# Optimization experiments

Hardware: AMD Instinct MI355X
Metric: run time of the kernel (lower is better)

## Reference

```python
import jax, jax.numpy as jnp
import numpy as np

B, S, D, H = 4, 2048, 1024, 16
HD = D // H  # head dim = 64


def setup_inputs() -> dict:
    key = jax.random.key(0)
    ks = jax.random.split(key, 9)
    scale = 1.0 / np.sqrt(D)
    return {
        "x": jax.random.normal(ks[0], (B, S, D), dtype=jnp.float32),
        "Wq": jax.random.normal(ks[1], (D, D), dtype=jnp.float32) * scale,
        "bq": jnp.zeros((D,), dtype=jnp.float32),
        "Wk": jax.random.normal(ks[2], (D, D), dtype=jnp.float32) * scale,
        "bk": jnp.zeros((D,), dtype=jnp.float32),
        "Wv": jax.random.normal(ks[3], (D, D), dtype=jnp.float32) * scale,
        "bv": jnp.zeros((D,), dtype=jnp.float32),
        "Wo": jax.random.normal(ks[4], (D, D), dtype=jnp.float32) * scale,
        "bo": jnp.zeros((D,), dtype=jnp.float32),
    }


def _split_heads(t):
    # [B,S,D] -> [B,H,S,HD]
    return t.reshape(t.shape[0], t.shape[1], H, HD).transpose(0, 2, 1, 3)


def reference(x, Wq, bq, Wk, bk, Wv, bv, Wo, bo):
    q = _split_heads(x @ Wq + bq)
    k = _split_heads(x @ Wk + bk)
    v = _split_heads(x @ Wv + bv)
    # scaled dot-product attention; scale by sqrt of key dim (= head dim)
    scores = jnp.einsum("bhqd,bhkd->bhqk", q, k) / jnp.sqrt(jnp.asarray(HD, q.dtype))
    weights = jax.nn.softmax(scores, axis=-1)
    attn = jnp.einsum("bhqk,bhkd->bhqd", weights, v)
    concat = attn.transpose(0, 2, 1, 3).reshape(x.shape[0], -1, D)
    out = concat @ Wo + bo
    return out, weights
```

## Files before the change

### kernel.cpp

```cpp
#include <hip/hip_runtime.h>
#include <cstddef>
#include <cstdint>

static constexpr int BB = 4;
static constexpr int SS = 2048;
static constexpr int DD = 1024;
static constexpr int HH = 16;
static constexpr int HDIM = 64;
static constexpr int MROWS = BB * SS;

typedef __attribute__((ext_vector_type(4))) float f32x4;
typedef __bf16 bf16x8 __attribute__((ext_vector_type(8)));
typedef __bf16 bf16x4 __attribute__((ext_vector_type(4)));

#define GLB_U32(p) ((const __attribute__((address_space(1))) uint32_t*)(p))
#define LDS_U32(p) ((__attribute__((address_space(3))) uint32_t*)(p))

__device__ __forceinline__ float fexp2(float x) {
#if __has_builtin(__builtin_amdgcn_exp2f)
    return __builtin_amdgcn_exp2f(x);
#else
    return exp2f(x);
#endif
}

__global__ __launch_bounds__(256) void cvt_x(const float* __restrict__ x,
                                             __bf16* __restrict__ xb)
{
    size_t i = ((size_t)blockIdx.x * 256 + threadIdx.x) * 8;
    float4 a = *reinterpret_cast<const float4*>(x + i);
    float4 b = *reinterpret_cast<const float4*>(x + i + 4);
    bf16x8 v;
    v[0] = (__bf16)a.x; v[1] = (__bf16)a.y; v[2] = (__bf16)a.z; v[3] = (__bf16)a.w;
    v[4] = (__bf16)b.x; v[5] = (__bf16)b.y; v[6] = (__bf16)b.z; v[7] = (__bf16)b.w;
    *reinterpret_cast<bf16x8*>(xb + i) = v;
}

__global__ __launch_bounds__(256) void transpose_w(
    const float* __restrict__ W0, const float* __restrict__ W1,
    const float* __restrict__ W2, const float* __restrict__ W3,
    __bf16* __restrict__ wt_base)
{
    const float* W = (blockIdx.z == 0) ? W0 : (blockIdx.z == 1) ? W1
                   : (blockIdx.z == 2) ? W2 : W3;
    __bf16* WT = wt_base + (size_t)blockIdx.z * 1048576;

    __shared__ float T[64][68];
    const int t = threadIdx.x;
    const int n0 = blockIdx.x * 64, k0 = blockIdx.y * 64;

#pragma unroll
    for (int it = 0; it < 4; ++it) {
        const int row = it * 16 + (t >> 4);
        const int col = (t & 15) * 4;
        float4 v = *reinterpret_cast<const float4*>(&W[(size_t)(k0 + row) * 1024 + n0 + col]);
        T[row][col + 0] = v.x; T[row][col + 1] = v.y;
        T[row][col + 2] = v.z; T[row][col + 3] = v.w;
    }
    __syncthreads();

#pragma unroll
    for (int it = 0; it < 2; ++it) {
        const int idx = it * 256 + t;
        const int n = idx >> 3, ch = idx & 7;
        bf16x8 v;
#pragma unroll
        for (int e = 0; e < 8; ++e) v[e] = (__bf16)T[ch * 8 + e][n];
        *reinterpret_cast<bf16x8*>(&WT[(size_t)(n0 + n) * 1024 + k0 + ch * 8]) = v;
    }
}

__global__ __launch_bounds__(256) void gemm_qkv(
    const __bf16* __restrict__ xb, const __bf16* __restrict__ wt,
    const float* __restrict__ bq, const float* __restrict__ bk,
    const float* __restrict__ bv,
    __bf16* __restrict__ qb, __bf16* __restrict__ kb, __bf16* __restrict__ vtb)
{
    __shared__ __bf16 AB[2 * 128 * 32];
    __bf16* At = AB;
    __bf16* Bt = AB + 4096;

    const int t = threadIdx.x;
    const int w = t >> 6, l = t & 63, l16 = l & 15, lg = l >> 4;
    const int m0 = blockIdx.x * 128;
    const int sel = blockIdx.y >> 3;
    const int n0 = (blockIdx.y & 7) * 128;
    const int wr = w >> 1, wc = w & 1;

    const __bf16* BT = wt + (size_t)sel * 1048576;
    const float* bias = (sel == 0) ? bq : (sel == 1) ? bk : bv;

    f32x4 acc[4][4] = {};

    for (int k0 = 0; k0 < 1024; k0 += 32) {
#pragma unroll
        for (int r = 0; r < 2; ++r) {
            const int cb = (w * 2 + r) * 64;
            const int ch = cb + l;
            const __bf16* srcA = xb + (size_t)(m0 + (ch >> 2)) * 1024 + k0 + (ch & 3) * 8;
            __builtin_amdgcn_global_load_lds(GLB_U32(srcA), LDS_U32(At + cb * 8), 16, 0, 0);
        }
#pragma unroll
        for (int r = 0; r < 2; ++r) {
            const int cb = (w * 2 + r) * 64;
            const int ch = cb + l;
            const __bf16* srcB = BT + (size_t)(n0 + (ch >> 2)) * 1024 + k0 + (ch & 3) * 8;
            __builtin_amdgcn_global_load_lds(GLB_U32(srcB), LDS_U32(Bt + cb * 8), 16, 0, 0);
        }
        __syncthreads();

        bf16x8 af[4], bf[4];
#pragma unroll
        for (int i = 0; i < 4; ++i) {
            af[i] = *reinterpret_cast<const bf16x8*>(At + (wr * 64 + i * 16 + l16) * 32 + lg * 8);
            bf[i] = *reinterpret_cast<const bf16x8*>(Bt + (wc * 64 + i * 16 + l16) * 32 + lg * 8);
        }
#pragma unroll
        for (int i = 0; i < 4; ++i)
#pragma unroll
            for (int j = 0; j < 4; ++j)
                acc[i][j] = __builtin_amdgcn_mfma_f32_16x16x32_bf16(af[i], bf[j], acc[i][j], 0, 0, 0);
        __syncthreads();
    }

    const float osc = (sel == 0) ? 0.18033688011112042f : 1.0f;

    if (sel < 2) {
        __bf16* Et = AB + w * 2048;
        __bf16* outp = (sel == 0) ? qb : kb;
#pragma unroll
        for (int j = 0; j < 4; ++j) {
            const float bvv = bias[n0 + wc * 64 + j * 16 + l16];
#pragma unroll
            for (int i = 0; i < 4; ++i)
#pragma unroll
                for (int r = 0; r < 4; ++r)
                    Et[(i * 16 + lg * 4 + r) * 24 + l16] =
                        (__bf16)((acc[i][j][r] + bvv) * osc);
#pragma unroll
            for (int it = 0; it < 2; ++it) {
                const int idx = it * 64 + l;
                const int ml = idx >> 1, ch = idx & 1;
                bf16x8 v = *(const bf16x8*)(Et + ml * 24 + ch * 8);
                const int M = m0 + wr * 64 + ml;
                const int N = n0 + wc * 64 + j * 16 + ch * 8;
                *(bf16x8*)(outp + (((size_t)(M >> 11) * HH + (N >> 6)) * SS
                                   + (M & 2047)) * HDIM + (N & 63)) = v;
            }
        }
    } else {
        __bf16* Et = AB + w * 2048;
#pragma unroll
        for (int j = 0; j < 4; ++j) {
            const float bvv = bias[n0 + wc * 64 + j * 16 + l16];
#pragma unroll
            for (int i = 0; i < 4; ++i)
#pragma unroll
                for (int r = 0; r < 4; ++r)
                    Et[l16 * 72 + i * 16 + lg * 4 + r] = (__bf16)(acc[i][j][r] + bvv);
#pragma unroll
            for (int it = 0; it < 2; ++it) {
                const int idx = it * 64 + l;
                const int row = idx >> 3, ch = idx & 7;
                bf16x8 v = *(const bf16x8*)(Et + row * 72 + ch * 8);
                const int N = n0 + wc * 64 + j * 16 + row;
                const int M = m0 + wr * 64 + ch * 8;
                *(bf16x8*)(vtb + (((size_t)(M >> 11) * HH + (N >> 6)) * HDIM
                                  + (N & 63)) * SS + (M & 2047)) = v;
            }
        }
    }
}

__global__ __launch_bounds__(256) void gemm_out(
    const __bf16* __restrict__ A, const __bf16* __restrict__ BT,
    const float* __restrict__ bias, float* __restrict__ C)
{
    __shared__ __bf16 AB[2 * 128 * 32];
    __bf16* At = AB;
    __bf16* Bt = AB + 4096;

    const int t = threadIdx.x;
    const int w = t >> 6, l = t & 63, l16 = l & 15, lg = l >> 4;
    const int m0 = blockIdx.x * 128, n0 = blockIdx.y * 128;
    const int wr = w >> 1, wc = w & 1;

    f32x4 acc[4][4] = {};

    for (int k0 = 0; k0 < 1024; k0 += 32) {
#pragma unroll
        for (int r = 0; r < 2; ++r) {
            const int cb = (w * 2 + r) * 64;
            const int ch = cb + l;
            const __bf16* srcA = A + (size_t)(m0 + (ch >> 2)) * 1024 + k0 + (ch & 3) * 8;
            __builtin_amdgcn_global_load_lds(GLB_U32(srcA), LDS_U32(At + cb * 8), 16, 0, 0);
        }
#pragma unroll
        for (int r = 0; r < 2; ++r) {
            const int cb = (w * 2 + r) * 64;
            const int ch = cb + l;
            const __bf16* srcB = BT + (size_t)(n0 + (ch >> 2)) * 1024 + k0 + (ch & 3) * 8;
            __builtin_amdgcn_global_load_lds(GLB_U32(srcB), LDS_U32(Bt + cb * 8), 16, 0, 0);
        }
        __syncthreads();

        bf16x8 af[4], bf[4];
#pragma unroll
        for (int i = 0; i < 4; ++i) {
            af[i] = *reinterpret_cast<const bf16x8*>(At + (wr * 64 + i * 16 + l16) * 32 + lg * 8);
            bf[i] = *reinterpret_cast<const bf16x8*>(Bt + (wc * 64 + i * 16 + l16) * 32 + lg * 8);
        }
#pragma unroll
        for (int i = 0; i < 4; ++i)
#pragma unroll
            for (int j = 0; j < 4; ++j)
                acc[i][j] = __builtin_amdgcn_mfma_f32_16x16x32_bf16(af[i], bf[j], acc[i][j], 0, 0, 0);
        __syncthreads();
    }

    float* Et = (float*)AB + w * 1024;
#pragma unroll
    for (int j = 0; j < 4; ++j) {
        const float bvv = bias[n0 + wc * 64 + j * 16 + l16];
#pragma unroll
        for (int i = 0; i < 4; ++i)
#pragma unroll
            for (int r = 0; r < 4; ++r)
                Et[(i * 16 + lg * 4 + r) * 16 + l16] = acc[i][j][r] + bvv;
#pragma unroll
        for (int it = 0; it < 4; ++it) {
            const int idx = it * 64 + l;
            const int ml = idx >> 2, ch = idx & 3;
            float4 v = *(const float4*)(Et + ml * 16 + ch * 4);
            const int M = m0 + wr * 64 + ml;
            const int N = n0 + wc * 64 + j * 16 + ch * 4;
            *(float4*)(C + (size_t)M * 1024 + N) = v;
        }
    }
}

__device__ __forceinline__ void stage64x64(const __bf16* __restrict__ g, int rstride,
                                           __bf16* lds, int t)
{
#pragma unroll
    for (int it = 0; it < 2; ++it) {
        const int i = it * 256 + t;
        const int r = i >> 3, j = i & 7;
        const __bf16* src = g + (size_t)r * rstride + ((j ^ (r & 7)) << 3);
        __builtin_amdgcn_global_load_lds(GLB_U32(src), LDS_U32(lds + i * 8), 16, 0, 0);
    }
}

__device__ __forceinline__ bf16x8 ldsF(const __bf16* buf, int row, int c0)
{
    return *(const bf16x8*)(buf + row * 64 + (((c0 >> 3) ^ (row & 7)) << 3));
}

__global__ __launch_bounds__(256, 4) void attn_fused(
    const __bf16* __restrict__ Qg, const __bf16* __restrict__ Kg,
    const __bf16* __restrict__ VTg, float* __restrict__ Wout,
    __bf16* __restrict__ attnb)
{
    __shared__ __bf16 Ksh[2][64 * 64];
    __shared__ __bf16 Vsh[2][64 * 64];
    __shared__ __bf16 Psh[4][16 * 64];

    const int t = threadIdx.x, w = t >> 6, l = t & 63, l16 = l & 15, lg = l >> 4;

    int bid = (int)blockIdx.x;
    bid = (bid & 7) * 256 + (bid >> 3);
    const int qt = bid & 31, bh = bid >> 5;
    const int qr = qt * 64 + w * 16;

    const __bf16* Qp = Qg + ((size_t)bh * SS + qr) * HDIM;
    const __bf16* Kp = Kg + (size_t)bh * SS * HDIM;
    const __bf16* Vp = VTg + (size_t)bh * HDIM * SS;

    const bf16x8 aq0 = *(const bf16x8*)(Qp + l16 * 64 + lg * 8);
    const bf16x8 aq1 = *(const bf16x8*)(Qp + l16 * 64 + 32 + lg * 8);

    char* pbase = (char*)&Psh[w][0];

    float ssum = 0.f;

    stage64x64(Kp, 64, Ksh[0], t);
    __syncthreads();

    for (int kt = 0; kt < 32; ++kt) {
        if (kt < 31) stage64x64(Kp + (kt + 1) * 4096, 64, Ksh[(kt + 1) & 1], t);
        const __bf16* kb = Ksh[kt & 1];

#pragma unroll
        for (int c4 = 0; c4 < 4; ++c4) {
            const bf16x8 b0 = ldsF(kb, c4 * 16 + l16, lg * 8);
            const bf16x8 b1 = ldsF(kb, c4 * 16 + l16, 32 + lg * 8);
            f32x4 a = {0.f, 0.f, 0.f, 0.f};
            a = __builtin_amdgcn_mfma_f32_16x16x32_bf16(b0, aq0, a, 0, 0, 0);
            a = __builtin_amdgcn_mfma_f32_16x16x32_bf16(b1, aq1, a, 0, 0, 0);
            ssum += (fexp2(a[0]) + fexp2(a[1])) + (fexp2(a[2]) + fexp2(a[3]));
        }
        __syncthreads();
    }

    stage64x64(Kp, 64, Ksh[0], t);
    stage64x64(Vp, SS, Vsh[0], t);

    ssum += __shfl_xor(ssum, 16);
    ssum += __shfl_xor(ssum, 32);
    const float linv = 1.0f / ssum;

    __syncthreads();

    f32x4 o[4] = {};
    float* wbase = Wout + ((size_t)bh * SS + qr + l16) * SS;

    for (int kt = 0; kt < 32; ++kt) {
        if (kt < 31) {
            stage64x64(Kp + (kt + 1) * 4096, 64, Ksh[(kt + 1) & 1], t);
            stage64x64(Vp + (kt + 1) * 64, SS, Vsh[(kt + 1) & 1], t);
        }
        const __bf16* kb = Ksh[kt & 1];
        const __bf16* vb = Vsh[kt & 1];

#pragma unroll
        for (int c4 = 0; c4 < 4; ++c4) {
            const bf16x8 b0 = ldsF(kb, c4 * 16 + l16, lg * 8);
            const bf16x8 b1 = ldsF(kb, c4 * 16 + l16, 32 + lg * 8);
            f32x4 a = {0.f, 0.f, 0.f, 0.f};
            a = __builtin_amdgcn_mfma_f32_16x16x32_bf16(b0, aq0, a, 0, 0, 0);
            a = __builtin_amdgcn_mfma_f32_16x16x32_bf16(b1, aq1, a, 0, 0, 0);
            f32x4 pv;
            pv[0] = fexp2(a[0]) * linv; pv[1] = fexp2(a[1]) * linv;
            pv[2] = fexp2(a[2]) * linv; pv[3] = fexp2(a[3]) * linv;
            __builtin_nontemporal_store(pv,
                (f32x4*)(wbase + kt * 64 + c4 * 16 + lg * 4));
            bf16x4 pk;
            pk[0] = (__bf16)pv[0]; pk[1] = (__bf16)pv[1];
            pk[2] = (__bf16)pv[2]; pk[3] = (__bf16)pv[3];
            const int off = l16 * 128 + ((c4 * 32 + lg * 8) ^ ((l16 & 7) << 4));
            *(bf16x4*)(pbase + off) = pk;
        }
        asm volatile("s_waitcnt lgkmcnt(0)" ::: "memory");
        __builtin_amdgcn_sched_barrier(0);

        bf16x8 pa[2];
#pragma unroll
        for (int kc = 0; kc < 2; ++kc) {
            const int off = l16 * 128 + ((kc * 64 + lg * 16) ^ ((l16 & 7) << 4));
            pa[kc] = *(const bf16x8*)(pbase + off);
        }
#pragma unroll
        for (int nt = 0; nt < 4; ++nt) {
            const bf16x8 bv0 = ldsF(vb, nt * 16 + l16, lg * 8);
            const bf16x8 bv1 = ldsF(vb, nt * 16 + l16, 32 + lg * 8);
            o[nt] = __builtin_amdgcn_mfma_f32_16x16x32_bf16(pa[0], bv0, o[nt], 0, 0, 0);
            o[nt] = __builtin_amdgcn_mfma_f32_16x16x32_bf16(pa[1], bv1, o[nt], 0, 0, 0);
        }

        if (kt < 31) {
            asm volatile("s_waitcnt vmcnt(4)" ::: "memory");
            __builtin_amdgcn_s_barrier();
        }
    }

    const int b = bh >> 4, h = bh & 15;
    __bf16* Pe = &Psh[w][0];
    asm volatile("s_waitcnt lgkmcnt(0)" ::: "memory");
    __builtin_amdgcn_sched_barrier(0);
#pragma unroll
    for (int nt = 0; nt < 4; ++nt)
#pragma unroll
        for (int r = 0; r < 4; ++r)
            Pe[(lg * 4 + r) * 64 + nt * 16 + l16] = (__bf16)o[nt][r];
    asm volatile("s_waitcnt lgkmcnt(0)" ::: "memory");
    __builtin_amdgcn_sched_barrier(0);
#pragma unroll
    for (int it = 0; it < 2; ++it) {
        const int idx = it * 64 + l;
        const int row = idx >> 3, ch = idx & 7;
        bf16x8 v = *(const bf16x8*)(Pe + row * 64 + ch * 8);
        *(bf16x8*)(attnb + ((size_t)b * SS + qr + row) * DD + h * 64 + ch * 8) = v;
    }
}

extern "C" void kernel_launch(void* const* d_in, const int* in_sizes, int n_in,
                              void* d_out, int out_size, void* d_ws, size_t ws_size,
                              hipStream_t stream)
{
    const float* x  = (const float*)d_in[0];
    const float* Wq = (const float*)d_in[1];
    const float* bq = (const float*)d_in[2];
    const float* Wk = (const float*)d_in[3];
    const float* bk = (const float*)d_in[4];
    const float* Wv = (const float*)d_in[5];
    const float* bv = (const float*)d_in[6];
    const float* Wo = (const float*)d_in[7];
    const float* bo = (const float*)d_in[8];

    float* out     = (float*)d_out;
    float* weights = out + (size_t)BB * SS * DD;

    __bf16* ws = (__bf16*)d_ws;
    const size_t NX = (size_t)MROWS * DD;
    __bf16* xb    = ws;
    __bf16* wtb   = xb + NX;
    __bf16* woT   = wtb + 3145728;
    __bf16* qb    = wtb + 4194304;
    __bf16* kb    = qb + NX;
    __bf16* vtb   = kb + NX;
    __bf16* attnb = vtb + NX;

    dim3 blk(256);

    cvt_x<<<dim3(4096), blk, 0, stream>>>(x, xb);
    transpose_w<<<dim3(16, 16, 4), blk, 0, stream>>>(Wq, Wk, Wv, Wo, wtb);

    gemm_qkv<<<dim3(64, 24), blk, 0, stream>>>(xb, wtb, bq, bk, bv, qb, kb, vtb);

    attn_fused<<<dim3(2048), blk, 0, stream>>>(qb, kb, vtb, weights, attnb);

    gemm_out<<<dim3(64, 8), blk, 0, stream>>>(attnb, woT, bo, out);
}
```

Before: 434.3 us.

## Process 32 query rows per wave to reuse staged K/V tiles

```diff
diff --git a/kernel.cpp b/kernel.cpp
--- a/kernel.cpp
+++ b/kernel.cpp
@@ -256,32 +256,36 @@
     return *(const bf16x8*)(buf + row * 64 + (((c0 >> 3) ^ (row & 7)) << 3));
 }
 
-__global__ __launch_bounds__(256, 4) void attn_fused(
+__global__ __launch_bounds__(256, 3) void attn_fused(
     const __bf16* __restrict__ Qg, const __bf16* __restrict__ Kg,
     const __bf16* __restrict__ VTg, float* __restrict__ Wout,
     __bf16* __restrict__ attnb)
 {
     __shared__ __bf16 Ksh[2][64 * 64];
     __shared__ __bf16 Vsh[2][64 * 64];
-    __shared__ __bf16 Psh[4][16 * 64];
+    __shared__ __bf16 Psh[4][32 * 64];
 
     const int t = threadIdx.x, w = t >> 6, l = t & 63, l16 = l & 15, lg = l >> 4;
 
     int bid = (int)blockIdx.x;
-    bid = (bid & 7) * 256 + (bid >> 3);
-    const int qt = bid & 31, bh = bid >> 5;
-    const int qr = qt * 64 + w * 16;
+    bid = (bid & 7) * 128 + (bid >> 3);
+    const int qt = bid & 15, bh = bid >> 4;
+    const int qr = qt * 128 + w * 32;
 
     const __bf16* Qp = Qg + ((size_t)bh * SS + qr) * HDIM;
     const __bf16* Kp = Kg + (size_t)bh * SS * HDIM;
     const __bf16* Vp = VTg + (size_t)bh * HDIM * SS;
 
-    const bf16x8 aq0 = *(const bf16x8*)(Qp + l16 * 64 + lg * 8);
-    const bf16x8 aq1 = *(const bf16x8*)(Qp + l16 * 64 + 32 + lg * 8);
+    bf16x8 aq[2][2];
+#pragma unroll
+    for (int s = 0; s < 2; ++s) {
+        aq[s][0] = *(const bf16x8*)(Qp + (s * 16 + l16) * 64 + lg * 8);
+        aq[s][1] = *(const bf16x8*)(Qp + (s * 16 + l16) * 64 + 32 + lg * 8);
+    }
 
     char* pbase = (char*)&Psh[w][0];
 
-    float ssum = 0.f;
+    float ssum0 = 0.f, ssum1 = 0.f;
 
     stage64x64(Kp, 64, Ksh[0], t);
     __syncthreads();
@@ -294,10 +298,13 @@
         for (int c4 = 0; c4 < 4; ++c4) {
             const bf16x8 b0 = ldsF(kb, c4 * 16 + l16, lg * 8);
             const bf16x8 b1 = ldsF(kb, c4 * 16 + l16, 32 + lg * 8);
-            f32x4 a = {0.f, 0.f, 0.f, 0.f};
-            a = __builtin_amdgcn_mfma_f32_16x16x32_bf16(b0, aq0, a, 0, 0, 0);
-            a = __builtin_amdgcn_mfma_f32_16x16x32_bf16(b1, aq1, a, 0, 0, 0);
-            ssum += (fexp2(a[0]) + fexp2(a[1])) + (fexp2(a[2]) + fexp2(a[3]));
+            f32x4 a0 = {0.f, 0.f, 0.f, 0.f}, a1 = {0.f, 0.f, 0.f, 0.f};
+            a0 = __builtin_amdgcn_mfma_f32_16x16x32_bf16(b0, aq[0][0], a0, 0, 0, 0);
+            a0 = __builtin_amdgcn_mfma_f32_16x16x32_bf16(b1, aq[0][1], a0, 0, 0, 0);
+            a1 = __builtin_amdgcn_mfma_f32_16x16x32_bf16(b0, aq[1][0], a1, 0, 0, 0);
+            a1 = __builtin_amdgcn_mfma_f32_16x16x32_bf16(b1, aq[1][1], a1, 0, 0, 0);
+            ssum0 += (fexp2(a0[0]) + fexp2(a0[1])) + (fexp2(a0[2]) + fexp2(a0[3]));
+            ssum1 += (fexp2(a1[0]) + fexp2(a1[1])) + (fexp2(a1[2]) + fexp2(a1[3]));
         }
         __syncthreads();
     }
@@ -305,14 +312,18 @@
     stage64x64(Kp, 64, Ksh[0], t);
     stage64x64(Vp, SS, Vsh[0], t);
 
-    ssum += __shfl_xor(ssum, 16);
-    ssum += __shfl_xor(ssum, 32);
-    const float linv = 1.0f / ssum;
+    ssum0 += __shfl_xor(ssum0, 16);
+    ssum0 += __shfl_xor(ssum0, 32);
+    ssum1 += __shfl_xor(ssum1, 16);
+    ssum1 += __shfl_xor(ssum1, 32);
+    const float linv0 = 1.0f / ssum0;
+    const float linv1 = 1.0f / ssum1;
 
     __syncthreads();
 
-    f32x4 o[4] = {};
-    float* wbase = Wout + ((size_t)bh * SS + qr + l16) * SS;
+    f32x4 o[2][4] = {};
+    float* wbase0 = Wout + ((size_t)bh * SS + qr + l16) * SS;
+    float* wbase1 = wbase0 + (size_t)16 * SS;
 
     for (int kt = 0; kt < 32; ++kt) {
         if (kt < 31) {
@@ -326,39 +337,55 @@
         for (int c4 = 0; c4 < 4; ++c4) {
             const bf16x8 b0 = ldsF(kb, c4 * 16 + l16, lg * 8);
             const bf16x8 b1 = ldsF(kb, c4 * 16 + l16, 32 + lg * 8);
-            f32x4 a = {0.f, 0.f, 0.f, 0.f};
-            a = __builtin_amdgcn_mfma_f32_16x16x32_bf16(b0, aq0, a, 0, 0, 0);
-            a = __builtin_amdgcn_mfma_f32_16x16x32_bf16(b1, aq1, a, 0, 0, 0);
-            f32x4 pv;
-            pv[0] = fexp2(a[0]) * linv; pv[1] = fexp2(a[1]) * linv;
-            pv[2] = fexp2(a[2]) * linv; pv[3] = fexp2(a[3]) * linv;
-            __builtin_nontemporal_store(pv,
-                (f32x4*)(wbase + kt * 64 + c4 * 16 + lg * 4));
-            bf16x4 pk;
-            pk[0] = (__bf16)pv[0]; pk[1] = (__bf16)pv[1];
-            pk[2] = (__bf16)pv[2]; pk[3] = (__bf16)pv[3];
-            const int off = l16 * 128 + ((c4 * 32 + lg * 8) ^ ((l16 & 7) << 4));
-            *(bf16x4*)(pbase + off) = pk;
+            f32x4 a0 = {0.f, 0.f, 0.f, 0.f}, a1 = {0.f, 0.f, 0.f, 0.f};
+            a0 = __builtin_amdgcn_mfma_f32_16x16x32_bf16(b0, aq[0][0], a0, 0, 0, 0);
+            a0 = __builtin_amdgcn_mfma_f32_16x16x32_bf16(b1, aq[0][1], a0, 0, 0, 0);
+            a1 = __builtin_amdgcn_mfma_f32_16x16x32_bf16(b0, aq[1][0], a1, 0, 0, 0);
+            a1 = __builtin_amdgcn_mfma_f32_16x16x32_bf16(b1, aq[1][1], a1, 0, 0, 0);
+
+            f32x4 pv0, pv1;
+            pv0[0] = fexp2(a0[0]) * linv0; pv0[1] = fexp2(a0[1]) * linv0;
+            pv0[2] = fexp2(a0[2]) * linv0; pv0[3] = fexp2(a0[3]) * linv0;
+            pv1[0] = fexp2(a1[0]) * linv1; pv1[1] = fexp2(a1[1]) * linv1;
+            pv1[2] = fexp2(a1[2]) * linv1; pv1[3] = fexp2(a1[3]) * linv1;
+            __builtin_nontemporal_store(pv0,
+                (f32x4*)(wbase0 + kt * 64 + c4 * 16 + lg * 4));
+            __builtin_nontemporal_store(pv1,
+                (f32x4*)(wbase1 + kt * 64 + c4 * 16 + lg * 4));
+
+            bf16x4 pk0, pk1;
+            pk0[0] = (__bf16)pv0[0]; pk0[1] = (__bf16)pv0[1];
+            pk0[2] = (__bf16)pv0[2]; pk0[3] = (__bf16)pv0[3];
+            pk1[0] = (__bf16)pv1[0]; pk1[1] = (__bf16)pv1[1];
+            pk1[2] = (__bf16)pv1[2]; pk1[3] = (__bf16)pv1[3];
+            const int swz = ((c4 * 32 + lg * 8) ^ ((l16 & 7) << 4));
+            *(bf16x4*)(pbase + l16 * 128 + swz) = pk0;
+            *(bf16x4*)(pbase + (16 + l16) * 128 + swz) = pk1;
         }
         asm volatile("s_waitcnt lgkmcnt(0)" ::: "memory");
         __builtin_amdgcn_sched_barrier(0);
 
-        bf16x8 pa[2];
-#pragma unroll
-        for (int kc = 0; kc < 2; ++kc) {
-            const int off = l16 * 128 + ((kc * 64 + lg * 16) ^ ((l16 & 7) << 4));
-            pa[kc] = *(const bf16x8*)(pbase + off);
-        }
+        bf16x8 pa[2][2];
+#pragma unroll
+        for (int s = 0; s < 2; ++s)
+#pragma unroll
+            for (int kc = 0; kc < 2; ++kc) {
+                const int off = (s * 16 + l16) * 128 +
+                                ((kc * 64 + lg * 16) ^ ((l16 & 7) << 4));
+                pa[s][kc] = *(const bf16x8*)(pbase + off);
+            }
 #pragma unroll
         for (int nt = 0; nt < 4; ++nt) {
             const bf16x8 bv0 = ldsF(vb, nt * 16 + l16, lg * 8);
             const bf16x8 bv1 = ldsF(vb, nt * 16 + l16, 32 + lg * 8);
-            o[nt] = __builtin_amdgcn_mfma_f32_16x16x32_bf16(pa[0], bv0, o[nt], 0, 0, 0);
-            o[nt] = __builtin_amdgcn_mfma_f32_16x16x32_bf16(pa[1], bv1, o[nt], 0, 0, 0);
+            o[0][nt] = __builtin_amdgcn_mfma_f32_16x16x32_bf16(pa[0][0], bv0, o[0][nt], 0, 0, 0);
+            o[0][nt] = __builtin_amdgcn_mfma_f32_16x16x32_bf16(pa[0][1], bv1, o[0][nt], 0, 0, 0);
+            o[1][nt] = __builtin_amdgcn_mfma_f32_16x16x32_bf16(pa[1][0], bv0, o[1][nt], 0, 0, 0);
+            o[1][nt] = __builtin_amdgcn_mfma_f32_16x16x32_bf16(pa[1][1], bv1, o[1][nt], 0, 0, 0);
         }
 
         if (kt < 31) {
-            asm volatile("s_waitcnt vmcnt(4)" ::: "memory");
+            asm volatile("s_waitcnt vmcnt(8)" ::: "memory");
             __builtin_amdgcn_s_barrier();
         }
     }
@@ -368,14 +395,16 @@
     asm volatile("s_waitcnt lgkmcnt(0)" ::: "memory");
     __builtin_amdgcn_sched_barrier(0);
 #pragma unroll
-    for (int nt = 0; nt < 4; ++nt)
-#pragma unroll
-        for (int r = 0; r < 4; ++r)
-            Pe[(lg * 4 + r) * 64 + nt * 16 + l16] = (__bf16)o[nt][r];
+    for (int s = 0; s < 2; ++s)
+#pragma unroll
+        for (int nt = 0; nt < 4; ++nt)
+#pragma unroll
+            for (int r = 0; r < 4; ++r)
+                Pe[(s * 16 + lg * 4 + r) * 64 + nt * 16 + l16] = (__bf16)o[s][nt][r];
     asm volatile("s_waitcnt lgkmcnt(0)" ::: "memory");
     __builtin_amdgcn_sched_barrier(0);
 #pragma unroll
-    for (int it = 0; it < 2; ++it) {
+    for (int it = 0; it < 4; ++it) {
         const int idx = it * 64 + l;
         const int row = idx >> 3, ch = idx & 7;
         bf16x8 v = *(const bf16x8*)(Pe + row * 64 + ch * 8);
@@ -417,7 +446,7 @@
 
     gemm_qkv<<<dim3(64, 24), blk, 0, stream>>>(xb, wtb, bq, bk, bv, qb, kb, vtb);
 
-    attn_fused<<<dim3(2048), blk, 0, stream>>>(qb, kb, vtb, weights, attnb);
+    attn_fused<<<dim3(1024), blk, 0, stream>>>(qb, kb, vtb, weights, attnb);
 
     gemm_out<<<dim3(64, 8), blk, 0, stream>>>(attnb, woT, bo, out);
 }
```

After: 474.7 us. 9.3% more time.

## Split softmax row-sum pass into a separate stats kernel with 32 rows per wave

Applied to the files above, without the earlier changes.

```diff
diff --git a/kernel.cpp b/kernel.cpp
--- a/kernel.cpp
+++ b/kernel.cpp
@@ -256,10 +256,68 @@
     return *(const bf16x8*)(buf + row * 64 + (((c0 >> 3) ^ (row & 7)) << 3));
 }
 
-__global__ __launch_bounds__(256, 4) void attn_fused(
+__global__ __launch_bounds__(256, 6) void attn_stats(
     const __bf16* __restrict__ Qg, const __bf16* __restrict__ Kg,
-    const __bf16* __restrict__ VTg, float* __restrict__ Wout,
-    __bf16* __restrict__ attnb)
+    float* __restrict__ linvArr)
+{
+    __shared__ __bf16 Ksh[2][64 * 64];
+
+    const int t = threadIdx.x, w = t >> 6, l = t & 63, l16 = l & 15, lg = l >> 4;
+
+    int bid = (int)blockIdx.x;
+    bid = (bid & 7) * 128 + (bid >> 3);
+    const int qt = bid & 15, bh = bid >> 4;
+    const int qr = qt * 128 + w * 32;
+
+    const __bf16* Qp = Qg + ((size_t)bh * SS + qr) * HDIM;
+    const __bf16* Kp = Kg + (size_t)bh * SS * HDIM;
+
+    bf16x8 aq[2][2];
+#pragma unroll
+    for (int s = 0; s < 2; ++s) {
+        aq[s][0] = *(const bf16x8*)(Qp + (s * 16 + l16) * 64 + lg * 8);
+        aq[s][1] = *(const bf16x8*)(Qp + (s * 16 + l16) * 64 + 32 + lg * 8);
+    }
+
+    float ssum0 = 0.f, ssum1 = 0.f;
+
+    stage64x64(Kp, 64, Ksh[0], t);
+    __syncthreads();
+
+    for (int kt = 0; kt < 32; ++kt) {
+        if (kt < 31) stage64x64(Kp + (kt + 1) * 4096, 64, Ksh[(kt + 1) & 1], t);
+        const __bf16* kb = Ksh[kt & 1];
+
+#pragma unroll
+        for (int c4 = 0; c4 < 4; ++c4) {
+            const bf16x8 b0 = ldsF(kb, c4 * 16 + l16, lg * 8);
+            const bf16x8 b1 = ldsF(kb, c4 * 16 + l16, 32 + lg * 8);
+            f32x4 a0 = {0.f, 0.f, 0.f, 0.f}, a1 = {0.f, 0.f, 0.f, 0.f};
+            a0 = __builtin_amdgcn_mfma_f32_16x16x32_bf16(b0, aq[0][0], a0, 0, 0, 0);
+            a0 = __builtin_amdgcn_mfma_f32_16x16x32_bf16(b1, aq[0][1], a0, 0, 0, 0);
+            a1 = __builtin_amdgcn_mfma_f32_16x16x32_bf16(b0, aq[1][0], a1, 0, 0, 0);
+            a1 = __builtin_amdgcn_mfma_f32_16x16x32_bf16(b1, aq[1][1], a1, 0, 0, 0);
+            ssum0 += (fexp2(a0[0]) + fexp2(a0[1])) + (fexp2(a0[2]) + fexp2(a0[3]));
+            ssum1 += (fexp2(a1[0]) + fexp2(a1[1])) + (fexp2(a1[2]) + fexp2(a1[3]));
+        }
+        __syncthreads();
+    }
+
+    ssum0 += __shfl_xor(ssum0, 16);
+    ssum0 += __shfl_xor(ssum0, 32);
+    ssum1 += __shfl_xor(ssum1, 16);
+    ssum1 += __shfl_xor(ssum1, 32);
+
+    if (lg == 0) {
+        linvArr[(size_t)bh * SS + qr + l16]      = 1.0f / ssum0;
+        linvArr[(size_t)bh * SS + qr + 16 + l16] = 1.0f / ssum1;
+    }
+}
+
+__global__ __launch_bounds__(256, 4) void attn_store(
+    const __bf16* __restrict__ Qg, const __bf16* __restrict__ Kg,
+    const __bf16* __restrict__ VTg, const float* __restrict__ linvArr,
+    float* __restrict__ Wout, __bf16* __restrict__ attnb)
 {
     __shared__ __bf16 Ksh[2][64 * 64];
     __shared__ __bf16 Vsh[2][64 * 64];
@@ -276,43 +334,18 @@
     const __bf16* Kp = Kg + (size_t)bh * SS * HDIM;
     const __bf16* Vp = VTg + (size_t)bh * HDIM * SS;
 
+    stage64x64(Kp, 64, Ksh[0], t);
+    stage64x64(Vp, SS, Vsh[0], t);
+
     const bf16x8 aq0 = *(const bf16x8*)(Qp + l16 * 64 + lg * 8);
     const bf16x8 aq1 = *(const bf16x8*)(Qp + l16 * 64 + 32 + lg * 8);
+    const float linv = linvArr[(size_t)bh * SS + qr + l16];
 
     char* pbase = (char*)&Psh[w][0];
-
-    float ssum = 0.f;
-
-    stage64x64(Kp, 64, Ksh[0], t);
-    __syncthreads();
-
-    for (int kt = 0; kt < 32; ++kt) {
-        if (kt < 31) stage64x64(Kp + (kt + 1) * 4096, 64, Ksh[(kt + 1) & 1], t);
-        const __bf16* kb = Ksh[kt & 1];
-
-#pragma unroll
-        for (int c4 = 0; c4 < 4; ++c4) {
-            const bf16x8 b0 = ldsF(kb, c4 * 16 + l16, lg * 8);
-            const bf16x8 b1 = ldsF(kb, c4 * 16 + l16, 32 + lg * 8);
-            f32x4 a = {0.f, 0.f, 0.f, 0.f};
-            a = __builtin_amdgcn_mfma_f32_16x16x32_bf16(b0, aq0, a, 0, 0, 0);
-            a = __builtin_amdgcn_mfma_f32_16x16x32_bf16(b1, aq1, a, 0, 0, 0);
-            ssum += (fexp2(a[0]) + fexp2(a[1])) + (fexp2(a[2]) + fexp2(a[3]));
-        }
-        __syncthreads();
-    }
-
-    stage64x64(Kp, 64, Ksh[0], t);
-    stage64x64(Vp, SS, Vsh[0], t);
-
-    ssum += __shfl_xor(ssum, 16);
-    ssum += __shfl_xor(ssum, 32);
-    const float linv = 1.0f / ssum;
-
-    __syncthreads();
-
     f32x4 o[4] = {};
     float* wbase = Wout + ((size_t)bh * SS + qr + l16) * SS;
+
+    __syncthreads();
 
     for (int kt = 0; kt < 32; ++kt) {
         if (kt < 31) {
@@ -409,6 +442,7 @@
     __bf16* kb    = qb + NX;
     __bf16* vtb   = kb + NX;
     __bf16* attnb = vtb + NX;
+    float*  linv  = (float*)(attnb + NX);
 
     dim3 blk(256);
 
@@ -417,7 +451,8 @@
 
     gemm_qkv<<<dim3(64, 24), blk, 0, stream>>>(xb, wtb, bq, bk, bv, qb, kb, vtb);
 
-    attn_fused<<<dim3(2048), blk, 0, stream>>>(qb, kb, vtb, weights, attnb);
+    attn_stats<<<dim3(1024), blk, 0, stream>>>(qb, kb, linv);
+    attn_store<<<dim3(2048), blk, 0, stream>>>(qb, kb, vtb, linv, weights, attnb);
 
     gemm_out<<<dim3(64, 8), blk, 0, stream>>>(attnb, woT, bo, out);
 }
```

Result: slower. 467.5 us (+7.6%).

## Process two query tiles per block, fusing B's row-sum pass into A's output pass

Applied to the files above, without the earlier changes.

```diff
diff --git a/kernel.cpp b/kernel.cpp
--- a/kernel.cpp
+++ b/kernel.cpp
@@ -256,7 +256,7 @@
     return *(const bf16x8*)(buf + row * 64 + (((c0 >> 3) ^ (row & 7)) << 3));
 }
 
-__global__ __launch_bounds__(256, 4) void attn_fused(
+__global__ __launch_bounds__(256) void attn_fused(
     const __bf16* __restrict__ Qg, const __bf16* __restrict__ Kg,
     const __bf16* __restrict__ VTg, float* __restrict__ Wout,
     __bf16* __restrict__ attnb)
@@ -268,20 +268,25 @@
     const int t = threadIdx.x, w = t >> 6, l = t & 63, l16 = l & 15, lg = l >> 4;
 
     int bid = (int)blockIdx.x;
-    bid = (bid & 7) * 256 + (bid >> 3);
-    const int qt = bid & 31, bh = bid >> 5;
-    const int qr = qt * 64 + w * 16;
-
-    const __bf16* Qp = Qg + ((size_t)bh * SS + qr) * HDIM;
+    bid = (bid & 7) * 128 + (bid >> 3);
+    const int qp = bid & 15, bh = bid >> 4;
+    const int qrA = qp * 128 + w * 16;
+    const int qrB = qrA + 64;
+
     const __bf16* Kp = Kg + (size_t)bh * SS * HDIM;
     const __bf16* Vp = VTg + (size_t)bh * HDIM * SS;
-
-    const bf16x8 aq0 = *(const bf16x8*)(Qp + l16 * 64 + lg * 8);
-    const bf16x8 aq1 = *(const bf16x8*)(Qp + l16 * 64 + 32 + lg * 8);
+    const __bf16* QpA = Qg + ((size_t)bh * SS + qrA) * HDIM;
+    const __bf16* QpB = Qg + ((size_t)bh * SS + qrB) * HDIM;
+
+    const bf16x8 aqA0 = *(const bf16x8*)(QpA + l16 * 64 + lg * 8);
+    const bf16x8 aqA1 = *(const bf16x8*)(QpA + l16 * 64 + 32 + lg * 8);
+    const bf16x8 aqB0 = *(const bf16x8*)(QpB + l16 * 64 + lg * 8);
+    const bf16x8 aqB1 = *(const bf16x8*)(QpB + l16 * 64 + 32 + lg * 8);
 
     char* pbase = (char*)&Psh[w][0];
-
-    float ssum = 0.f;
+    const int b = bh >> 4, h = bh & 15;
+
+    float ssumA = 0.f;
 
     stage64x64(Kp, 64, Ksh[0], t);
     __syncthreads();
@@ -295,9 +300,9 @@
             const bf16x8 b0 = ldsF(kb, c4 * 16 + l16, lg * 8);
             const bf16x8 b1 = ldsF(kb, c4 * 16 + l16, 32 + lg * 8);
             f32x4 a = {0.f, 0.f, 0.f, 0.f};
-            a = __builtin_amdgcn_mfma_f32_16x16x32_bf16(b0, aq0, a, 0, 0, 0);
-            a = __builtin_amdgcn_mfma_f32_16x16x32_bf16(b1, aq1, a, 0, 0, 0);
-            ssum += (fexp2(a[0]) + fexp2(a[1])) + (fexp2(a[2]) + fexp2(a[3]));
+            a = __builtin_amdgcn_mfma_f32_16x16x32_bf16(b0, aqA0, a, 0, 0, 0);
+            a = __builtin_amdgcn_mfma_f32_16x16x32_bf16(b1, aqA1, a, 0, 0, 0);
+            ssumA += (fexp2(a[0]) + fexp2(a[1])) + (fexp2(a[2]) + fexp2(a[3]));
         }
         __syncthreads();
     }
@@ -305,14 +310,15 @@
     stage64x64(Kp, 64, Ksh[0], t);
     stage64x64(Vp, SS, Vsh[0], t);
 
-    ssum += __shfl_xor(ssum, 16);
-    ssum += __shfl_xor(ssum, 32);
-    const float linv = 1.0f / ssum;
+    ssumA += __shfl_xor(ssumA, 16);
+    ssumA += __shfl_xor(ssumA, 32);
+    const float linvA = 1.0f / ssumA;
 
     __syncthreads();
 
     f32x4 o[4] = {};
-    float* wbase = Wout + ((size_t)bh * SS + qr + l16) * SS;
+    float ssumB = 0.f;
+    float* wbaseA = Wout + ((size_t)bh * SS + qrA + l16) * SS;
 
     for (int kt = 0; kt < 32; ++kt) {
         if (kt < 31) {
@@ -327,18 +333,22 @@
             const bf16x8 b0 = ldsF(kb, c4 * 16 + l16, lg * 8);
             const bf16x8 b1 = ldsF(kb, c4 * 16 + l16, 32 + lg * 8);
             f32x4 a = {0.f, 0.f, 0.f, 0.f};
-            a = __builtin_amdgcn_mfma_f32_16x16x32_bf16(b0, aq0, a, 0, 0, 0);
-            a = __builtin_amdgcn_mfma_f32_16x16x32_bf16(b1, aq1, a, 0, 0, 0);
+            a = __builtin_amdgcn_mfma_f32_16x16x32_bf16(b0, aqA0, a, 0, 0, 0);
+            a = __builtin_amdgcn_mfma_f32_16x16x32_bf16(b1, aqA1, a, 0, 0, 0);
             f32x4 pv;
-            pv[0] = fexp2(a[0]) * linv; pv[1] = fexp2(a[1]) * linv;
-            pv[2] = fexp2(a[2]) * linv; pv[3] = fexp2(a[3]) * linv;
+            pv[0] = fexp2(a[0]) * linvA; pv[1] = fexp2(a[1]) * linvA;
+            pv[2] = fexp2(a[2]) * linvA; pv[3] = fexp2(a[3]) * linvA;
             __builtin_nontemporal_store(pv,
-                (f32x4*)(wbase + kt * 64 + c4 * 16 + lg * 4));
+                (f32x4*)(wbaseA + kt * 64 + c4 * 16 + lg * 4));
             bf16x4 pk;
             pk[0] = (__bf16)pv[0]; pk[1] = (__bf16)pv[1];
             pk[2] = (__bf16)pv[2]; pk[3] = (__bf16)pv[3];
             const int off = l16 * 128 + ((c4 * 32 + lg * 8) ^ ((l16 & 7) << 4));
             *(bf16x4*)(pbase + off) = pk;
+            f32x4 s = {0.f, 0.f, 0.f, 0.f};
+            s = __builtin_amdgcn_mfma_f32_16x16x32_bf16(b0, aqB0, s, 0, 0, 0);
+            s = __builtin_amdgcn_mfma_f32_16x16x32_bf16(b1, aqB1, s, 0, 0, 0);
+            ssumB += (fexp2(s[0]) + fexp2(s[1])) + (fexp2(s[2]) + fexp2(s[3]));
         }
         asm volatile("s_waitcnt lgkmcnt(0)" ::: "memory");
         __builtin_amdgcn_sched_barrier(0);
@@ -363,23 +373,105 @@
         }
     }
 
-    const int b = bh >> 4, h = bh & 15;
-    __bf16* Pe = &Psh[w][0];
-    asm volatile("s_waitcnt lgkmcnt(0)" ::: "memory");
-    __builtin_amdgcn_sched_barrier(0);
-#pragma unroll
-    for (int nt = 0; nt < 4; ++nt)
-#pragma unroll
-        for (int r = 0; r < 4; ++r)
-            Pe[(lg * 4 + r) * 64 + nt * 16 + l16] = (__bf16)o[nt][r];
-    asm volatile("s_waitcnt lgkmcnt(0)" ::: "memory");
-    __builtin_amdgcn_sched_barrier(0);
-#pragma unroll
-    for (int it = 0; it < 2; ++it) {
-        const int idx = it * 64 + l;
-        const int row = idx >> 3, ch = idx & 7;
-        bf16x8 v = *(const bf16x8*)(Pe + row * 64 + ch * 8);
-        *(bf16x8*)(attnb + ((size_t)b * SS + qr + row) * DD + h * 64 + ch * 8) = v;
+    stage64x64(Kp, 64, Ksh[0], t);
+    stage64x64(Vp, SS, Vsh[0], t);
+
+    ssumB += __shfl_xor(ssumB, 16);
+    ssumB += __shfl_xor(ssumB, 32);
+    const float linvB = 1.0f / ssumB;
+
+    {
+        __bf16* Pe = &Psh[w][0];
+        asm volatile("s_waitcnt lgkmcnt(0)" ::: "memory");
+        __builtin_amdgcn_sched_barrier(0);
+#pragma unroll
+        for (int nt = 0; nt < 4; ++nt)
+#pragma unroll
+            for (int r = 0; r < 4; ++r)
+                Pe[(lg * 4 + r) * 64 + nt * 16 + l16] = (__bf16)o[nt][r];
+        asm volatile("s_waitcnt lgkmcnt(0)" ::: "memory");
+        __builtin_amdgcn_sched_barrier(0);
+#pragma unroll
+        for (int it = 0; it < 2; ++it) {
+            const int idx = it * 64 + l;
+            const int row = idx >> 3, ch = idx & 7;
+            bf16x8 v = *(const bf16x8*)(Pe + row * 64 + ch * 8);
+            *(bf16x8*)(attnb + ((size_t)b * SS + qrA + row) * DD + h * 64 + ch * 8) = v;
+        }
+#pragma unroll
+        for (int nt = 0; nt < 4; ++nt) o[nt] = (f32x4){0.f, 0.f, 0.f, 0.f};
+    }
+    __syncthreads();
+
+    float* wbaseB = Wout + ((size_t)bh * SS + qrB + l16) * SS;
+
+    for (int kt = 0; kt < 32; ++kt) {
+        if (kt < 31) {
+            stage64x64(Kp + (kt + 1) * 4096, 64, Ksh[(kt + 1) & 1], t);
+            stage64x64(Vp + (kt + 1) * 64, SS, Vsh[(kt + 1) & 1], t);
+        }
+        const __bf16* kb = Ksh[kt & 1];
+        const __bf16* vb = Vsh[kt & 1];
+
+#pragma unroll
+        for (int c4 = 0; c4 < 4; ++c4) {
+            const bf16x8 b0 = ldsF(kb, c4 * 16 + l16, lg * 8);
+            const bf16x8 b1 = ldsF(kb, c4 * 16 + l16, 32 + lg * 8);
+            f32x4 a = {0.f, 0.f, 0.f, 0.f};
+            a = __builtin_amdgcn_mfma_f32_16x16x32_bf16(b0, aqB0, a, 0, 0, 0);
+            a = __builtin_amdgcn_mfma_f32_16x16x32_bf16(b1, aqB1, a, 0, 0, 0);
+            f32x4 pv;
+            pv[0] = fexp2(a[0]) * linvB; pv[1] = fexp2(a[1]) * linvB;
+            pv[2] = fexp2(a[2]) * linvB; pv[3] = fexp2(a[3]) * linvB;
+            __builtin_nontemporal_store(pv,
+                (f32x4*)(wbaseB + kt * 64 + c4 * 16 + lg * 4));
+            bf16x4 pk;
+            pk[0] = (__bf16)pv[0]; pk[1] = (__bf16)pv[1];
+            pk[2] = (__bf16)pv[2]; pk[3] = (__bf16)pv[3];
+            const int off = l16 * 128 + ((c4 * 32 + lg * 8) ^ ((l16 & 7) << 4));
+            *(bf16x4*)(pbase + off) = pk;
+        }
+        asm volatile("s_waitcnt lgkmcnt(0)" ::: "memory");
+        __builtin_amdgcn_sched_barrier(0);
+
+        bf16x8 pa[2];
+#pragma unroll
+        for (int kc = 0; kc < 2; ++kc) {
+            const int off = l16 * 128 + ((kc * 64 + lg * 16) ^ ((l16 & 7) << 4));
+            pa[kc] = *(const bf16x8*)(pbase + off);
+        }
+#pragma unroll
+        for (int nt = 0; nt < 4; ++nt) {
+            const bf16x8 bv0 = ldsF(vb, nt * 16 + l16, lg * 8);
+            const bf16x8 bv1 = ldsF(vb, nt * 16 + l16, 32 + lg * 8);
+            o[nt] = __builtin_amdgcn_mfma_f32_16x16x32_bf16(pa[0], bv0, o[nt], 0, 0, 0);
+            o[nt] = __builtin_amdgcn_mfma_f32_16x16x32_bf16(pa[1], bv1, o[nt], 0, 0, 0);
+        }
+
+        if (kt < 31) {
+            asm volatile("s_waitcnt vmcnt(4)" ::: "memory");
+            __builtin_amdgcn_s_barrier();
+        }
+    }
+
+    {
+        __bf16* Pe = &Psh[w][0];
+        asm volatile("s_waitcnt lgkmcnt(0)" ::: "memory");
+        __builtin_amdgcn_sched_barrier(0);
+#pragma unroll
+        for (int nt = 0; nt < 4; ++nt)
+#pragma unroll
+            for (int r = 0; r < 4; ++r)
+                Pe[(lg * 4 + r) * 64 + nt * 16 + l16] = (__bf16)o[nt][r];
+        asm volatile("s_waitcnt lgkmcnt(0)" ::: "memory");
+        __builtin_amdgcn_sched_barrier(0);
+#pragma unroll
+        for (int it = 0; it < 2; ++it) {
+            const int idx = it * 64 + l;
+            const int row = idx >> 3, ch = idx & 7;
+            bf16x8 v = *(const bf16x8*)(Pe + row * 64 + ch * 8);
+            *(bf16x8*)(attnb + ((size_t)b * SS + qrB + row) * DD + h * 64 + ch * 8) = v;
+        }
     }
 }
 
@@ -417,7 +509,7 @@
 
     gemm_qkv<<<dim3(64, 24), blk, 0, stream>>>(xb, wtb, bq, bk, bv, qb, kb, vtb);
 
-    attn_fused<<<dim3(2048), blk, 0, stream>>>(qb, kb, vtb, weights, attnb);
+    attn_fused<<<dim3(1024), blk, 0, stream>>>(qb, kb, vtb, weights, attnb);
 
     gemm_out<<<dim3(64, 8), blk, 0, stream>>>(attnb, woT, bo, out);
 }
```

Result: slower. 460.3 us (+6.0%).
